# Performance work log

Hardware: AMD Instinct MI355X
Metric: run time of the kernel (lower is better)

Reference implementation:

```python
import jax, jax.numpy as jnp
import numpy as np

N_TOKENS = 8192   # batch*seq
D_IN = 4096
D_OUT = 4096
RANK = 64


def setup_inputs() -> dict:
    key = jax.random.key(0)
    k_x, k_s, k_u, k_d, k_q = jax.random.split(key, 5)
    x = jax.random.normal(k_x, (N_TOKENS, D_IN), dtype=jnp.float32)
    scales = jax.random.uniform(k_s, (D_OUT, 1), dtype=jnp.float32)
    U = jax.random.normal(k_u, (D_OUT, RANK), dtype=jnp.float32)
    D = jax.random.normal(k_d, (RANK, D_IN), dtype=jnp.float32)
    Q = jax.random.randint(k_q, (D_OUT, D_IN), 0, 127, dtype=jnp.int32)
    return {"x": x, "scales": scales, "U": U, "D": D, "Q": Q}


def reference(x, scales, U, D, Q):
    # Dequantize: Wdq[o, i] = Q[o, i] * scales[o]  -> fp32 [D_OUT, D_IN]
    Wdq = Q.astype(jnp.float32) * scales
    # Main GEMM: [N, D_IN] @ [D_IN, D_OUT]
    main = x @ Wdq.T
    # Low-rank adapter: x @ D.T -> [N, RANK], then @ U.T -> [N, D_OUT]
    adapt = (x @ D.T) @ U.T
    return main + adapt
```

## Files before the change

### kernel.cpp

```cpp
#include <hip/hip_runtime.h>
#include <hip/hip_fp16.h>
#include <cstdint>

#define M_TOK 8192
#define K_IN  4096
#define N_OUT 4096
#define RANK  64
#define KSPLIT 8

typedef _Float16 f16x8 __attribute__((ext_vector_type(8)));
typedef _Float16 f16x4 __attribute__((ext_vector_type(4)));
typedef float    f32x4 __attribute__((ext_vector_type(4)));

__device__ __forceinline__ void gld_lds16(const void* g, void* l) {
    __builtin_amdgcn_global_load_lds(
        (const __attribute__((address_space(1))) void*)g,
        (__attribute__((address_space(3))) void*)l,
        16, 0, 0);
}

__global__ void k_cvt_f32_f16(const float4* __restrict__ in,
                              f16x4* __restrict__ out, int n4) {
    int i = blockIdx.x * 256 + threadIdx.x;
    if (i >= n4) return;
    float4 v = in[i];
    f16x4 r;
    r[0] = (_Float16)v.x; r[1] = (_Float16)v.y;
    r[2] = (_Float16)v.z; r[3] = (_Float16)v.w;
    out[i] = r;
}

__global__ void k_cvt_w8(const int4* __restrict__ Q, const float* __restrict__ s,
                         f16x8* __restrict__ W) {
    int i = blockIdx.x * 256 + threadIdx.x;
    float sc = s[i >> 9];
    int4 q0 = Q[2 * i], q1 = Q[2 * i + 1];
    f16x8 r;
    r[0] = (_Float16)(q0.x * sc); r[1] = (_Float16)(q0.y * sc);
    r[2] = (_Float16)(q0.z * sc); r[3] = (_Float16)(q0.w * sc);
    r[4] = (_Float16)(q1.x * sc); r[5] = (_Float16)(q1.y * sc);
    r[6] = (_Float16)(q1.z * sc); r[7] = (_Float16)(q1.w * sc);
    W[i] = r;
}

__global__ __launch_bounds__(256)
void k_t_fused(const float* __restrict__ X, const _Float16* __restrict__ Dh,
               _Float16* __restrict__ Xh, float* __restrict__ T32) {
    __shared__ _Float16 Xs[64 * 32];
    __shared__ _Float16 Ds[64 * 32];
    const int tid = threadIdx.x, wave = tid >> 6, lane = tid & 63;
    const int row0 = blockIdx.x * 64;
    const int kbase = blockIdx.y * (K_IN / KSPLIT);
    const int lr = tid >> 2, lk = (tid & 3) * 8;
    const int rr = lane >> 2, c8 = (lane & 3) * 8;
    const int fm = lane & 15, fk = (lane >> 4) * 8;
    f32x4 acc[4] = {};

    for (int kk = 0; kk < K_IN / KSPLIT; kk += 32) {
        const int k0 = kbase + kk;
        const float* gx = X + (size_t)(row0 + lr) * K_IN + k0 + lk;
        float4 v0 = *(const float4*)gx;
        float4 v1 = *(const float4*)(gx + 4);
        f16x8 h;
        h[0] = (_Float16)v0.x; h[1] = (_Float16)v0.y;
        h[2] = (_Float16)v0.z; h[3] = (_Float16)v0.w;
        h[4] = (_Float16)v1.x; h[5] = (_Float16)v1.y;
        h[6] = (_Float16)v1.z; h[7] = (_Float16)v1.w;
        *(f16x8*)(Xh + (size_t)(row0 + lr) * K_IN + k0 + lk) = h;
        *(f16x8*)&Xs[lr * 32 + lk] = h;
        gld_lds16(Dh + (size_t)(wave * 16 + rr) * K_IN + k0 + c8,
                  Ds + wave * 16 * 32);
        __syncthreads();
        f16x8 a = *(const f16x8*)&Xs[(wave * 16 + fm) * 32 + fk];
#pragma unroll
        for (int n = 0; n < 4; n++) {
            f16x8 b = *(const f16x8*)&Ds[(n * 16 + fm) * 32 + fk];
            acc[n] = __builtin_amdgcn_mfma_f32_16x16x32_f16(a, b, acc[n], 0, 0, 0);
        }
        __syncthreads();
    }
#pragma unroll
    for (int n = 0; n < 4; n++)
#pragma unroll
        for (int r = 0; r < 4; r++) {
            int row = row0 + wave * 16 + (lane >> 4) * 4 + r;
            int col = n * 16 + (lane & 15);
            T32[((size_t)blockIdx.y * M_TOK + row) * RANK + col] = acc[n][r];
        }
}

__global__ void k_reduce_t(const float* __restrict__ T32,
                           _Float16* __restrict__ Th) {
    int i = blockIdx.x * 256 + threadIdx.x;
    float s = 0.f;
#pragma unroll
    for (int c = 0; c < KSPLIT; c++)
        s += T32[(size_t)c * M_TOK * RANK + i];
    Th[i] = (_Float16)s;
}

__global__ __launch_bounds__(256)
void k_main(const _Float16* __restrict__ A, const _Float16* __restrict__ B,
            const _Float16* __restrict__ T, const _Float16* __restrict__ U,
            float* __restrict__ C) {
    __shared__ _Float16 As[128 * 32];
    __shared__ _Float16 Bs[128 * 32];
    const int tid = threadIdx.x, wave = tid >> 6, lane = tid & 63;
    const int bx = blockIdx.x, by = blockIdx.y;
    const int wr = wave >> 1, wc = wave & 1;
    const int rr = lane >> 2, c8 = (lane & 3) * 8;
    const int fm = lane & 15, fk = (lane >> 4) * 8;
    const int arow0 = by * 128, brow0 = bx * 128;

    f32x4 acc[4][4] = {};

    auto step = [&](const _Float16* Ab, size_t lda,
                    const _Float16* Bb, size_t ldb, int k0) {
        const _Float16* ga = Ab + (size_t)(arow0 + wave * 32 + rr) * lda + k0 + c8;
        gld_lds16(ga,            As + wave * 32 * 32);
        gld_lds16(ga + 16 * lda, As + wave * 32 * 32 + 16 * 32);
        const _Float16* gb = Bb + (size_t)(brow0 + wave * 32 + rr) * ldb + k0 + c8;
        gld_lds16(gb,            Bs + wave * 32 * 32);
        gld_lds16(gb + 16 * ldb, Bs + wave * 32 * 32 + 16 * 32);
        __syncthreads();
        f16x8 a[4], b[4];
#pragma unroll
        for (int m = 0; m < 4; m++)
            a[m] = *(const f16x8*)&As[(wr * 64 + m * 16 + fm) * 32 + fk];
#pragma unroll
        for (int n = 0; n < 4; n++)
            b[n] = *(const f16x8*)&Bs[(wc * 64 + n * 16 + fm) * 32 + fk];
#pragma unroll
        for (int m = 0; m < 4; m++)
#pragma unroll
            for (int n = 0; n < 4; n++)
                acc[m][n] = __builtin_amdgcn_mfma_f32_16x16x32_f16(
                    a[m], b[n], acc[m][n], 0, 0, 0);
        __syncthreads();
    };

    for (int k0 = 0; k0 < K_IN; k0 += 32)
        step(A, K_IN, B, K_IN, k0);
    step(T, RANK, U, RANK, 0);
    step(T, RANK, U, RANK, 32);

#pragma unroll
    for (int m = 0; m < 4; m++) {
        int row = by * 128 + wr * 64 + m * 16 + (lane >> 4) * 4;
#pragma unroll
        for (int n = 0; n < 4; n++) {
            int col = bx * 128 + wc * 64 + n * 16 + (lane & 15);
            float* cp = C + (size_t)row * N_OUT + col;
#pragma unroll
            for (int r = 0; r < 4; r++)
                cp[(size_t)r * N_OUT] = acc[m][n][r];
        }
    }
}

__global__ void fb_t(const float* __restrict__ x, const float* __restrict__ Dm,
                     float* __restrict__ t) {
    int n = blockIdx.x, r = threadIdx.x;
    const float* xr = x + (size_t)n * K_IN;
    const float* dr = Dm + (size_t)r * K_IN;
    float s = 0.f;
    for (int k = 0; k < K_IN; k++) s += xr[k] * dr[k];
    t[n * RANK + r] = s;
}

__global__ void fb_main(const float* __restrict__ x, const float* __restrict__ scales,
                        const float* __restrict__ U, const int* __restrict__ Q,
                        const float* __restrict__ t, float* __restrict__ out) {
    size_t i = (size_t)blockIdx.x * 256 + threadIdx.x;
    int n = (int)(i >> 12), o = (int)(i & 4095);
    const float* xr = x + (size_t)n * K_IN;
    const int* qr = Q + (size_t)o * K_IN;
    float s = 0.f;
    for (int k = 0; k < K_IN; k++) s += xr[k] * (float)qr[k];
    float a = 0.f;
    const float* tr = t + (size_t)n * RANK;
    const float* ur = U + (size_t)o * RANK;
    for (int r = 0; r < RANK; r++) a += tr[r] * ur[r];
    out[i] = scales[o] * s + a;
}

extern "C" void kernel_launch(void* const* d_in, const int* in_sizes, int n_in,
                              void* d_out, int out_size, void* d_ws, size_t ws_size,
                              hipStream_t stream) {
    const float* x      = (const float*)d_in[0];
    const float* scales = (const float*)d_in[1];
    const float* U      = (const float*)d_in[2];
    const float* D      = (const float*)d_in[3];
    const int*   Q      = (const int*)d_in[4];
    float* out = (float*)d_out;

    const size_t SZ_X   = (size_t)M_TOK * K_IN * 2;
    const size_t SZ_W   = (size_t)N_OUT * K_IN * 2;
    const size_t SZ_U   = (size_t)N_OUT * RANK * 2;
    const size_t SZ_D   = (size_t)RANK * K_IN * 2;
    const size_t SZ_T   = (size_t)M_TOK * RANK * 2;
    const size_t SZ_T32 = (size_t)KSPLIT * M_TOK * RANK * 4;
    const size_t NEED   = SZ_X + SZ_W + SZ_U + SZ_D + SZ_T + SZ_T32;

    if (ws_size >= NEED) {
        char* w = (char*)d_ws;
        _Float16* xh  = (_Float16*)w; w += SZ_X;
        _Float16* Wh  = (_Float16*)w; w += SZ_W;
        _Float16* Uh  = (_Float16*)w; w += SZ_U;
        _Float16* Dh  = (_Float16*)w; w += SZ_D;
        _Float16* Th  = (_Float16*)w; w += SZ_T;
        float*    T32 = (float*)w;

        k_cvt_f32_f16<<<256, 256, 0, stream>>>((const float4*)U, (f16x4*)Uh,
                                               N_OUT * RANK / 4);
        k_cvt_f32_f16<<<256, 256, 0, stream>>>((const float4*)D, (f16x4*)Dh,
                                               RANK * K_IN / 4);
        k_t_fused<<<dim3(M_TOK / 64, KSPLIT), 256, 0, stream>>>(x, Dh, xh, T32);
        k_reduce_t<<<M_TOK * RANK / 256, 256, 0, stream>>>(T32, Th);
        k_cvt_w8<<<N_OUT * K_IN / 8 / 256, 256, 0, stream>>>((const int4*)Q,
                                                             scales, (f16x8*)Wh);
        k_main<<<dim3(N_OUT / 128, M_TOK / 128), 256, 0, stream>>>(xh, Wh, Th, Uh, out);
    } else {
        float* t32 = (float*)d_ws;
        fb_t<<<M_TOK, RANK, 0, stream>>>(x, D, t32);
        fb_main<<<(int)((size_t)M_TOK * N_OUT / 256), 256, 0, stream>>>(
            x, scales, U, Q, t32, out);
    }
}
```

Measured before the change: 642.8 us.

## Split x conversion into separate kernel and make low-rank projection barrier-free

Un-fuses the fp32→fp16 conversion of x from the low-rank projection kernel into a standalone vectorized conversion kernel. The projection kernel now loads MFMA fragments directly from global memory with no LDS staging and no __syncthreads, and its loop is unrolled. This is meant to remove barrier stalls and LDS traffic in the T computation. In exchange, the fp16 copy of x is written and then read back from global memory, and each wave does less coalesced direct global loads, re-reading D without any LDS sharing.

```diff
diff --git a/kernel.cpp b/kernel.cpp
--- a/kernel.cpp
+++ b/kernel.cpp
@@ -27,6 +27,18 @@
     f16x4 r;
     r[0] = (_Float16)v.x; r[1] = (_Float16)v.y;
     r[2] = (_Float16)v.z; r[3] = (_Float16)v.w;
+    out[i] = r;
+}
+
+__global__ void k_cvt_x8(const float4* __restrict__ in,
+                         f16x8* __restrict__ out) {
+    int i = blockIdx.x * 256 + threadIdx.x;
+    float4 v0 = in[2 * i], v1 = in[2 * i + 1];
+    f16x8 r;
+    r[0] = (_Float16)v0.x; r[1] = (_Float16)v0.y;
+    r[2] = (_Float16)v0.z; r[3] = (_Float16)v0.w;
+    r[4] = (_Float16)v1.x; r[5] = (_Float16)v1.y;
+    r[6] = (_Float16)v1.z; r[7] = (_Float16)v1.w;
     out[i] = r;
 }
 
@@ -44,47 +56,34 @@
 }
 
 __global__ __launch_bounds__(256)
-void k_t_fused(const float* __restrict__ X, const _Float16* __restrict__ Dh,
-               _Float16* __restrict__ Xh, float* __restrict__ T32) {
-    __shared__ _Float16 Xs[64 * 32];
-    __shared__ _Float16 Ds[64 * 32];
+void k_t_nb(const _Float16* __restrict__ Xh, const _Float16* __restrict__ Dh,
+            float* __restrict__ T32) {
     const int tid = threadIdx.x, wave = tid >> 6, lane = tid & 63;
-    const int row0 = blockIdx.x * 64;
+    const int row0 = blockIdx.x * 64 + wave * 16;
     const int kbase = blockIdx.y * (K_IN / KSPLIT);
-    const int lr = tid >> 2, lk = (tid & 3) * 8;
-    const int rr = lane >> 2, c8 = (lane & 3) * 8;
     const int fm = lane & 15, fk = (lane >> 4) * 8;
     f32x4 acc[4] = {};
-
+    const _Float16* ap = Xh + (size_t)(row0 + fm) * K_IN + kbase + fk;
+    const _Float16* bp = Dh + (size_t)fm * K_IN + kbase + fk;
+
+#pragma unroll 4
     for (int kk = 0; kk < K_IN / KSPLIT; kk += 32) {
-        const int k0 = kbase + kk;
-        const float* gx = X + (size_t)(row0 + lr) * K_IN + k0 + lk;
-        float4 v0 = *(const float4*)gx;
-        float4 v1 = *(const float4*)(gx + 4);
-        f16x8 h;
-        h[0] = (_Float16)v0.x; h[1] = (_Float16)v0.y;
-        h[2] = (_Float16)v0.z; h[3] = (_Float16)v0.w;
-        h[4] = (_Float16)v1.x; h[5] = (_Float16)v1.y;
-        h[6] = (_Float16)v1.z; h[7] = (_Float16)v1.w;
-        *(f16x8*)(Xh + (size_t)(row0 + lr) * K_IN + k0 + lk) = h;
-        *(f16x8*)&Xs[lr * 32 + lk] = h;
-        gld_lds16(Dh + (size_t)(wave * 16 + rr) * K_IN + k0 + c8,
-                  Ds + wave * 16 * 32);
-        __syncthreads();
-        f16x8 a = *(const f16x8*)&Xs[(wave * 16 + fm) * 32 + fk];
-#pragma unroll
-        for (int n = 0; n < 4; n++) {
-            f16x8 b = *(const f16x8*)&Ds[(n * 16 + fm) * 32 + fk];
-            acc[n] = __builtin_amdgcn_mfma_f32_16x16x32_f16(a, b, acc[n], 0, 0, 0);
-        }
-        __syncthreads();
+        f16x8 a  = *(const f16x8*)(ap + kk);
+        f16x8 b0 = *(const f16x8*)(bp + kk);
+        f16x8 b1 = *(const f16x8*)(bp + 16 * K_IN + kk);
+        f16x8 b2 = *(const f16x8*)(bp + 32 * K_IN + kk);
+        f16x8 b3 = *(const f16x8*)(bp + 48 * K_IN + kk);
+        acc[0] = __builtin_amdgcn_mfma_f32_16x16x32_f16(a, b0, acc[0], 0, 0, 0);
+        acc[1] = __builtin_amdgcn_mfma_f32_16x16x32_f16(a, b1, acc[1], 0, 0, 0);
+        acc[2] = __builtin_amdgcn_mfma_f32_16x16x32_f16(a, b2, acc[2], 0, 0, 0);
+        acc[3] = __builtin_amdgcn_mfma_f32_16x16x32_f16(a, b3, acc[3], 0, 0, 0);
     }
 #pragma unroll
     for (int n = 0; n < 4; n++)
 #pragma unroll
         for (int r = 0; r < 4; r++) {
-            int row = row0 + wave * 16 + (lane >> 4) * 4 + r;
-            int col = n * 16 + (lane & 15);
+            int row = row0 + (lane >> 4) * 4 + r;
+            int col = n * 16 + fm;
             T32[((size_t)blockIdx.y * M_TOK + row) * RANK + col] = acc[n][r];
         }
 }
@@ -215,7 +214,9 @@
                                                N_OUT * RANK / 4);
         k_cvt_f32_f16<<<256, 256, 0, stream>>>((const float4*)D, (f16x4*)Dh,
                                                RANK * K_IN / 4);
-        k_t_fused<<<dim3(M_TOK / 64, KSPLIT), 256, 0, stream>>>(x, Dh, xh, T32);
+        k_cvt_x8<<<M_TOK * K_IN / 8 / 256, 256, 0, stream>>>((const float4*)x,
+                                                             (f16x8*)xh);
+        k_t_nb<<<dim3(M_TOK / 64, KSPLIT), 256, 0, stream>>>(xh, Dh, T32);
         k_reduce_t<<<M_TOK * RANK / 256, 256, 0, stream>>>(T32, Th);
         k_cvt_w8<<<N_OUT * K_IN / 8 / 256, 256, 0, stream>>>((const int4*)Q,
                                                              scales, (f16x8*)Wh);
```

Result: no change. 651.5 us (+1.4%).
